# Kernel tuning notes

Measured on AMD Instinct MI355X. Metric: run time of the kernel, lower is better.

## Reference

```python
import jax, jax.numpy as jnp
import numpy as np

B, IN, H, T = 4096, 1024, 1024, 12
TIME_PENALTY = 0.01
PONDER_EPS = 0.01


def lstm_cell(x, h, c, Wih, Whh, bih, bhh):
    # PyTorch LSTMCell: gates ordered i, f, g, o
    g = x @ Wih.T + bih + h @ Whh.T + bhh  # [B, 4H]
    i, f, gg, o = jnp.split(g, 4, axis=1)
    i = jax.nn.sigmoid(i)
    f = jax.nn.sigmoid(f)
    gg = jnp.tanh(gg)
    o = jax.nn.sigmoid(o)
    c_new = f * c + i * gg
    h_new = o * jnp.tanh(c_new)
    return h_new, c_new


def setup_inputs() -> dict:
    key = jax.random.key(0)
    ks = jax.random.split(key, 12)
    k1 = 1.0 / np.sqrt(H)
    u = lambda k, shape: jax.random.uniform(k, shape, jnp.float32, -k1, k1)
    return {
        "inputs": jax.random.normal(ks[0], (B, IN), jnp.float32),
        "W_ih1": u(ks[1], (4 * H, IN + 1)),
        "W_hh1": u(ks[2], (4 * H, H)),
        "b_ih1": u(ks[3], (4 * H,)),
        "b_hh1": u(ks[4], (4 * H,)),
        "W_ih2": u(ks[5], (4 * H, H)),
        "W_hh2": u(ks[6], (4 * H, H)),
        "b_ih2": u(ks[7], (4 * H,)),
        "b_hh2": u(ks[8], (4 * H,)),
        "W_halt": u(ks[9], (1, H)),
        "b_halt": jnp.full((1,), -1.0, jnp.float32),  # initial_halting_bias
    }


def reference(inputs, W_ih1, W_hh1, b_ih1, b_hh1, W_ih2, W_hh2, b_ih2, b_hh2, W_halt, b_halt):
    batch = inputs.shape[0]
    budget = jnp.float32(1.0 - PONDER_EPS)

    h1 = jnp.zeros((batch, H), jnp.float32)
    c1 = jnp.zeros((batch, H), jnp.float32)
    h2 = jnp.zeros((batch, H), jnp.float32)
    c2 = jnp.zeros((batch, H), jnp.float32)
    halt_accum = jnp.zeros((batch, 1), jnp.float32)
    acc_out = jnp.zeros((batch, H), jnp.float32)
    acc_rem = jnp.zeros((batch, 1), jnp.float32)
    ponder_steps = jnp.zeros((batch,), jnp.float32)
    cont = jnp.ones((batch, 1), bool)
    is_first = jnp.array(True)

    def step(carry, _):
        h1, c1, h2, c2, halt_accum, acc_out, acc_rem, ponder_steps, cont, is_first = carry
        active = jnp.any(cont)  # mimic torch's early break: inactive steps are no-ops
        flag = jnp.where(is_first, 1.0, 0.0) * jnp.ones((batch, 1), jnp.float32)
        x = jnp.concatenate([inputs, flag], axis=1)
        h1n, c1n = lstm_cell(x, h1, c1, W_ih1, W_hh1, b_ih1, b_hh1)
        act = jax.nn.relu(h1n)
        h2n, c2n = lstm_cell(act, h2, c2, W_ih2, W_hh2, b_ih2, b_hh2)
        step_halt = jax.nn.sigmoid(h2n @ W_halt.T + b_halt)  # [B,1]
        cont_f = cont.astype(jnp.float32)
        masked_halt = step_halt * cont_f
        halt_n = halt_accum + masked_halt
        ending = (halt_n > budget) & cont
        cont_n = cont & jnp.logical_not(ending)
        masked_rem = ending.astype(jnp.float32) * (1.0 - halt_n)
        acc_out_n = acc_out + (masked_halt + masked_rem) * h2n
        acc_rem_n = acc_rem + masked_halt
        ponder_n = ponder_steps + cont_n[:, 0].astype(jnp.float32)
        sel = lambda new, old: jnp.where(active, new, old)
        carry_n = (sel(h1n, h1), sel(c1n, c1), sel(h2n, h2), sel(c2n, c2),
                   sel(halt_n, halt_accum), sel(acc_out_n, acc_out),
                   sel(acc_rem_n, acc_rem), sel(ponder_n, ponder_steps),
                   jnp.where(active, cont_n, cont),
                   is_first & jnp.logical_not(active))
        return carry_n, None

    carry = (h1, c1, h2, c2, halt_accum, acc_out, acc_rem, ponder_steps, cont, is_first)
    carry, _ = jax.lax.scan(step, carry, None, length=T)
    h1, c1, h2, c2, halt_accum, acc_out, acc_rem, ponder_steps, cont, _ = carry

    # for-else branch: samples still continuing after time_limit get the remainder
    acc_out = acc_out + cont.astype(jnp.float32) * (1.0 - halt_accum) * h2
    ponder_cost = -1.0 * TIME_PENALTY * jnp.mean(acc_rem)
    return acc_out, h1, c1, h2, c2, ponder_cost, ponder_steps
```

## Files before the change

kernel.cpp:

```cpp
#include <hip/hip_runtime.h>
#include <cstdint>
#include <cstddef>


typedef _Float16 f16;
typedef f16   f16x8 __attribute__((ext_vector_type(8)));
typedef f16   f16x4 __attribute__((ext_vector_type(4)));
typedef float f32x4 __attribute__((ext_vector_type(4)));

#define TSTEPS 12

#define O_ACC   0u
#define O_H1    4194304u
#define O_C1    8388608u
#define O_H2    12582912u
#define O_C2    16777216u
#define O_PCOST 20971520u
#define O_PSTEP 20971521u

#define WS_C1    (size_t)(0u)
#define WS_C2    ((size_t)16u<<20)
#define WS_H1HI0 ((size_t)32u<<20)
#define WS_H1HI1 ((size_t)40u<<20)
#define WS_H1LO0 ((size_t)48u<<20)
#define WS_H1LO1 ((size_t)56u<<20)
#define WS_H2HI0 ((size_t)64u<<20)
#define WS_H2HI1 ((size_t)72u<<20)
#define WS_H2LO0 ((size_t)80u<<20)
#define WS_H2LO1 ((size_t)88u<<20)
#define WS_ACTHI ((size_t)96u<<20)
#define WS_ACTLO ((size_t)104u<<20)
#define WS_MISC  ((size_t)112u<<20)

#define SEC_AHI 0
#define SEC_ALO 16384
#define SEC_BHI 32768
#define SEC_BLO 49152
#define BUFSZ   65536

__device__ __forceinline__ float sigmoidf_(float x) { return 1.0f / (1.0f + expf(-x)); }

__device__ __forceinline__ void glds16(const void* g, void* l) {
    __builtin_amdgcn_global_load_lds(
        (const __attribute__((address_space(1))) unsigned int*)g,
        (__attribute__((address_space(3))) unsigned int*)l, 16, 0, 0);
}

__device__ __forceinline__ void block_tile(int& m0, int& hc0) {
    const int bid = blockIdx.x;
    const int lid = (bid & 7) * 32 + (bid >> 3);
    m0  = (lid & 15) * 256;
    hc0 = (lid >> 4) * 64;
}

template<bool B_PAIR>
__device__ __forceinline__ void pass256(
    const f16* __restrict__ Ahi, const f16* __restrict__ Alo,
    const f16* __restrict__ Bhi, const f16* __restrict__ Blo,
    const float* __restrict__ Bf32,
    int m0, int hc0, f32x4 (&acc)[8][4], char* sm)
{
    const int tid = threadIdx.x, lane = tid & 63, wid = tid >> 6;
    const int wm  = (wid >> 2) * 128;
    const int wnb = wid & 3;
    const int l15 = lane & 15, lk = lane >> 4;
    const int rswz16 = (lk ^ (l15 & 3)) << 4;

    int aoff[8], boff[4];
#pragma unroll
    for (int mf = 0; mf < 8; ++mf) aoff[mf] = (wm + mf * 16 + l15) * 64 + rswz16;
#pragma unroll
    for (int nf = 0; nf < 4; ++nf) boff[nf] = (wnb * 64 + nf * 16 + l15) * 64 + rswz16;

    constexpr int NOPS = B_PAIR ? 8 : 4;
    const f16* gsrc[NOPS];
    int ldst[NOPS];
    {
        const int gl_d = lane >> 2;
        const int swzel = ((lane & 3) ^ (gl_d & 3)) * 8;
#pragma unroll
        for (int i = 0; i < NOPS; ++i) {
            const int o = wid * NOPS + i;
            const int sec = o >> 4, j = o & 15;
            const f16* base;
            size_t row;
            if (sec <= 1) { base = (sec == 0) ? Ahi : Alo; row = (size_t)(m0 + 16 * j + gl_d); }
            else {
                base = (sec == 2) ? Bhi : Blo;
                row = (size_t)((j & 3) * 1024 + hc0 + (j >> 2) * 16 + gl_d);
            }
            gsrc[i] = base + row * 1024 + swzel;
            ldst[i] = sec * 16384 + j * 1024 + lane * 16;
        }
    }

    const int blv = tid >> 1;
    const float* bsrc = nullptr;
    float4 breg[4];
    if constexpr (!B_PAIR) {
        const int wrow = ((blv >> 4) & 3) * 1024 + hc0 + (blv >> 6) * 16 + (blv & 15);
        bsrc = Bf32 + (size_t)wrow * 1024 + (tid & 1) * 16;
    }

    auto issue = [&](int i, int kt, char* buf) {
        glds16(gsrc[i] + kt * 32, buf + ldst[i]);
    };
    auto loadB = [&](int kt) {
#pragma unroll
        for (int i = 0; i < 4; ++i) breg[i] = *(const float4*)(bsrc + kt * 32 + i * 4);
    };
    auto writeB = [&](char* buf) {
#pragma unroll
        for (int i = 0; i < 4; ++i) {
            const float4 v = breg[i];
            const f16 s0 = (f16)v.x, s1 = (f16)v.y, s2 = (f16)v.z, s3 = (f16)v.w;
            const f16x4 hv = {s0, s1, s2, s3};
            const f16x4 lw = {(f16)(v.x - (float)s0), (f16)(v.y - (float)s1),
                              (f16)(v.z - (float)s2), (f16)(v.w - (float)s3)};
            const int s = (((tid & 1) * 2 + (i >> 1)) ^ (blv & 3));
            const int off = blv * 64 + (s << 4) + (i & 1) * 8;
            *(f16x4*)(buf + SEC_BHI + off) = hv;
            *(f16x4*)(buf + SEC_BLO + off) = lw;
        }
    };

    constexpr int IST_P[5] = {0, 3, 6, 8, 8};
    constexpr int IST_M[5] = {0, 2, 3, 4, 4};

#pragma unroll
    for (int i = 0; i < NOPS; ++i) issue(i, 0, sm);
    if constexpr (!B_PAIR) {
        loadB(0);
        asm volatile("s_waitcnt vmcnt(0)" ::: "memory");
        writeB(sm);
    }
    asm volatile("s_waitcnt vmcnt(0) lgkmcnt(0)" ::: "memory");
    __builtin_amdgcn_s_barrier();
    asm volatile("" ::: "memory");

    int cur = 0;
#pragma unroll 1
    for (int kt = 0; kt < 32; ++kt) {
        char* bc = sm + cur * BUFSZ;
        char* bn = sm + (cur ^ 1) * BUFSZ;
        const bool pre = (kt < 31);
        f16x8 bh[4], bl[4];
#pragma unroll
        for (int p = 0; p < 4; ++p) {
            f16x8 ah0 = *(const f16x8*)(bc + SEC_AHI + aoff[2 * p]);
            f16x8 ah1 = *(const f16x8*)(bc + SEC_AHI + aoff[2 * p + 1]);
            f16x8 al0 = *(const f16x8*)(bc + SEC_ALO + aoff[2 * p]);
            f16x8 al1 = *(const f16x8*)(bc + SEC_ALO + aoff[2 * p + 1]);
            if (p == 0) {
#pragma unroll
                for (int nf = 0; nf < 4; ++nf) {
                    bh[nf] = *(const f16x8*)(bc + SEC_BHI + boff[nf]);
                    bl[nf] = *(const f16x8*)(bc + SEC_BLO + boff[nf]);
                }
            }
            if (pre) {
                if constexpr (B_PAIR) {
#pragma unroll
                    for (int i = IST_P[p]; i < IST_P[p + 1]; ++i) issue(i, kt + 1, bn);
                } else {
#pragma unroll
                    for (int i = IST_M[p]; i < IST_M[p + 1]; ++i) issue(i, kt + 1, bn);
                    if (p == 0) loadB(kt + 1);
                }
            }
            __builtin_amdgcn_s_barrier();
#pragma unroll
            for (int i = 0; i < 2; ++i) {
                const f16x8 xh = i ? ah1 : ah0;
                const f16x8 xl = i ? al1 : al0;
#pragma unroll
                for (int nf = 0; nf < 4; ++nf) {
                    acc[2 * p + i][nf] = __builtin_amdgcn_mfma_f32_16x16x32_f16(xh, bh[nf], acc[2 * p + i][nf], 0, 0, 0);
                    acc[2 * p + i][nf] = __builtin_amdgcn_mfma_f32_16x16x32_f16(xh, bl[nf], acc[2 * p + i][nf], 0, 0, 0);
                    acc[2 * p + i][nf] = __builtin_amdgcn_mfma_f32_16x16x32_f16(xl, bh[nf], acc[2 * p + i][nf], 0, 0, 0);
                }
            }
            if (p < 3) __builtin_amdgcn_s_barrier();
        }
        asm volatile("s_waitcnt vmcnt(0)" ::: "memory");
        if constexpr (!B_PAIR) { if (pre) writeB(bn); }
        asm volatile("s_waitcnt lgkmcnt(0)" ::: "memory");
        __builtin_amdgcn_s_barrier();
        asm volatile("" ::: "memory");
        cur ^= 1;
    }
}

__global__ __launch_bounds__(512) void k_z1(
    const f16* __restrict__ xhi, const f16* __restrict__ xlo,
    const f16* __restrict__ W1hi, const f16* __restrict__ W1lo,
    const float* __restrict__ bih1, const float* __restrict__ bhh1,
    float* __restrict__ Z1)
{
    __shared__ __align__(16) char sm[2 * BUFSZ];
    int m0, hc0; block_tile(m0, hc0);
    f32x4 acc[8][4];
#pragma unroll
    for (int a = 0; a < 8; ++a)
#pragma unroll
        for (int b = 0; b < 4; ++b) acc[a][b] = (f32x4){0.f, 0.f, 0.f, 0.f};
    pass256<true>(xhi, xlo, W1hi, W1lo, nullptr, m0, hc0, acc, sm);

    const int tid = threadIdx.x, lane = tid & 63, wid = tid >> 6;
    const int wm = (wid >> 2) * 128, wnb = wid & 3, l15 = lane & 15, lk = lane >> 4;
    const int hc = hc0 + wnb * 16 + l15;
#pragma unroll
    for (int mf = 0; mf < 8; ++mf)
#pragma unroll
        for (int r = 0; r < 4; ++r) {
            const int row = m0 + wm + mf * 16 + lk * 4 + r;
#pragma unroll
            for (int g = 0; g < 4; ++g) {
                const int R = g * 1024 + hc;
                Z1[(size_t)row * 4096 + R] = acc[mf][g][r] + bih1[R] + bhh1[R];
            }
        }
}

__global__ __launch_bounds__(512) void k_stepA(
    const float* __restrict__ Z1, const float* __restrict__ Whh1,
    const f16* __restrict__ h1hi_in, const f16* __restrict__ h1lo_in,
    const float* __restrict__ flagcol, float* __restrict__ c1,
    f16* __restrict__ h1hi_out, f16* __restrict__ h1lo_out,
    f16* __restrict__ acthi, f16* __restrict__ actlo,
    const unsigned* __restrict__ cnt_prev, int step)
{
    if (step > 0 && cnt_prev[0] == 0u) return;
    __shared__ __align__(16) char sm[2 * BUFSZ];
    int m0, hc0; block_tile(m0, hc0);
    f32x4 acc[8][4];
#pragma unroll
    for (int a = 0; a < 8; ++a)
#pragma unroll
        for (int b = 0; b < 4; ++b) acc[a][b] = (f32x4){0.f, 0.f, 0.f, 0.f};
    if (step > 0)
        pass256<false>(h1hi_in, h1lo_in, nullptr, nullptr, Whh1, m0, hc0, acc, sm);

    const int tid = threadIdx.x, lane = tid & 63, wid = tid >> 6;
    const int wm = (wid >> 2) * 128, wnb = wid & 3, l15 = lane & 15, lk = lane >> 4;
    const int hc = hc0 + wnb * 16 + l15;
#pragma unroll
    for (int mf = 0; mf < 8; ++mf)
#pragma unroll
        for (int r = 0; r < 4; ++r) {
            const int row = m0 + wm + mf * 16 + lk * 4 + r;
            float p[4];
#pragma unroll
            for (int g = 0; g < 4; ++g) {
                const int R = g * 1024 + hc;
                p[g] = acc[mf][g][r] + Z1[(size_t)row * 4096 + R];
                if (step == 0) p[g] += flagcol[R];
            }
            const float ig = sigmoidf_(p[0]);
            const float fg = sigmoidf_(p[1]);
            const float gg = tanhf(p[2]);
            const float og = sigmoidf_(p[3]);
            const int idx = row * 1024 + hc;
            const float cn = fg * c1[idx] + ig * gg;
            c1[idx] = cn;
            const float h = og * tanhf(cn);
            const f16 hh = (f16)h;
            const f16 hl = (f16)(h - (float)hh);
            h1hi_out[idx] = hh; h1lo_out[idx] = hl;
            const bool pos = h > 0.0f;
            acthi[idx] = pos ? hh : (f16)0.0f;
            actlo[idx] = pos ? hl : (f16)0.0f;
        }
}

__global__ __launch_bounds__(512) void k_stepB(
    const f16* __restrict__ acthi, const f16* __restrict__ actlo,
    const float* __restrict__ Wih2,
    const f16* __restrict__ h2hi_in, const f16* __restrict__ h2lo_in,
    const float* __restrict__ Whh2,
    const float* __restrict__ bih2, const float* __restrict__ bhh2,
    float* __restrict__ c2, f16* __restrict__ h2hi_out, f16* __restrict__ h2lo_out,
    const unsigned* __restrict__ cnt_prev, int step)
{
    if (step > 0 && cnt_prev[0] == 0u) return;
    __shared__ __align__(16) char sm[2 * BUFSZ];
    int m0, hc0; block_tile(m0, hc0);
    f32x4 acc[8][4];
#pragma unroll
    for (int a = 0; a < 8; ++a)
#pragma unroll
        for (int b = 0; b < 4; ++b) acc[a][b] = (f32x4){0.f, 0.f, 0.f, 0.f};
    pass256<false>(acthi, actlo, nullptr, nullptr, Wih2, m0, hc0, acc, sm);
    if (step > 0)
        pass256<false>(h2hi_in, h2lo_in, nullptr, nullptr, Whh2, m0, hc0, acc, sm);

    const int tid = threadIdx.x, lane = tid & 63, wid = tid >> 6;
    const int wm = (wid >> 2) * 128, wnb = wid & 3, l15 = lane & 15, lk = lane >> 4;
    const int hc = hc0 + wnb * 16 + l15;
#pragma unroll
    for (int mf = 0; mf < 8; ++mf)
#pragma unroll
        for (int r = 0; r < 4; ++r) {
            const int row = m0 + wm + mf * 16 + lk * 4 + r;
            float p[4];
#pragma unroll
            for (int g = 0; g < 4; ++g) {
                const int R = g * 1024 + hc;
                p[g] = acc[mf][g][r] + bih2[R] + bhh2[R];
            }
            const float ig = sigmoidf_(p[0]);
            const float fg = sigmoidf_(p[1]);
            const float gg = tanhf(p[2]);
            const float og = sigmoidf_(p[3]);
            const int idx = row * 1024 + hc;
            const float cn = fg * c2[idx] + ig * gg;
            c2[idx] = cn;
            const float h = og * tanhf(cn);
            const f16 hh = (f16)h;
            h2hi_out[idx] = hh;
            h2lo_out[idx] = (f16)(h - (float)hh);
        }
}

__global__ __launch_bounds__(256) void k_halt(
    const f16* __restrict__ h2hi, const f16* __restrict__ h2lo,
    const float* __restrict__ Whalt, const float* __restrict__ bhalt,
    float* __restrict__ halt, float* __restrict__ cont, float* __restrict__ coef,
    float* __restrict__ ponder_out, unsigned* __restrict__ ctrl,
    const unsigned* __restrict__ cnt_prev, int step)
{
    if (step > 0 && cnt_prev[0] == 0u) return;
    const int lane = threadIdx.x & 63;
    const int b = blockIdx.x * 4 + (threadIdx.x >> 6);
    const size_t base = (size_t)b * 1024;
    float sum = 0.0f;
    for (int k = lane; k < 1024; k += 64)
        sum += ((float)h2hi[base + k] + (float)h2lo[base + k]) * Whalt[k];
#pragma unroll
    for (int off = 32; off > 0; off >>= 1) sum += __shfl_down(sum, off, 64);
    if (lane == 0) {
        const float sh = sigmoidf_(sum + bhalt[0]);
        float co = 0.0f;
        if (cont[b] != 0.0f) {
            const float hn = halt[b] + sh;
            const bool ending = hn > 0.99f;
            co = sh + (ending ? (1.0f - hn) : 0.0f);
            halt[b] = hn;
            if (!ending) {
                ponder_out[b] += 1.0f;
                atomicAdd(&ctrl[step], 1u);
            } else {
                cont[b] = 0.0f;
            }
        }
        coef[b] = co;
        if (b == 0) ctrl[12] = (unsigned)(step + 1);
    }
}

__global__ __launch_bounds__(256) void k_accum(
    const f16* __restrict__ h2hi, const f16* __restrict__ h2lo,
    const float* __restrict__ coef, float* __restrict__ acc_out,
    const unsigned* __restrict__ cnt_prev, int step)
{
    if (step > 0 && cnt_prev[0] == 0u) return;
    const int b = blockIdx.x;
    const float co = coef[b];
    if (co == 0.0f) return;
    const size_t base = (size_t)b * 1024;
    const int i = threadIdx.x;
    const f16x4 hv = *(const f16x4*)(h2hi + base + i * 4);
    const f16x4 lv = *(const f16x4*)(h2lo + base + i * 4);
    float4* dst = (float4*)(acc_out + base);
    float4 d = dst[i];
    d.x = fmaf(co, (float)hv[0] + (float)lv[0], d.x);
    d.y = fmaf(co, (float)hv[1] + (float)lv[1], d.y);
    d.z = fmaf(co, (float)hv[2] + (float)lv[2], d.z);
    d.w = fmaf(co, (float)hv[3] + (float)lv[3], d.w);
    dst[i] = d;
}

__global__ __launch_bounds__(256) void k_small_init(
    float* __restrict__ halt, float* __restrict__ cont,
    float* __restrict__ ponder_out, unsigned* __restrict__ ctrl)
{
    const int b = blockIdx.x * 256 + threadIdx.x;
    if (b < 4096) { halt[b] = 0.0f; cont[b] = 1.0f; ponder_out[b] = 0.0f; }
    if (b < 16) ctrl[b] = 0u;
}

__global__ __launch_bounds__(256) void k_split_flat(
    const float* __restrict__ src, f16* __restrict__ hi, f16* __restrict__ lo)
{
    const size_t i = ((size_t)blockIdx.x * 256 + threadIdx.x) * 4;
    const float4 v = *(const float4*)(src + i);
    const f16 s0 = (f16)v.x, s1 = (f16)v.y, s2 = (f16)v.z, s3 = (f16)v.w;
    const f16x4 hv = {s0, s1, s2, s3};
    const f16x4 lw = {(f16)(v.x - (float)s0), (f16)(v.y - (float)s1),
                      (f16)(v.z - (float)s2), (f16)(v.w - (float)s3)};
    *(f16x4*)(hi + i) = hv;
    *(f16x4*)(lo + i) = lw;
}

__global__ __launch_bounds__(256) void k_split_wih1(
    const float* __restrict__ src, f16* __restrict__ hi, f16* __restrict__ lo,
    float* __restrict__ flagcol)
{
    const int t = blockIdx.x * 256 + threadIdx.x;
    const int row = t >> 8, c4 = (t & 255) << 2;
    const float* s = src + (size_t)row * 1025 + c4;
    const float v0 = s[0], v1 = s[1], v2 = s[2], v3 = s[3];
    const f16 s0 = (f16)v0, s1 = (f16)v1, s2 = (f16)v2, s3 = (f16)v3;
    const f16x4 hv = {s0, s1, s2, s3};
    const f16x4 lw = {(f16)(v0 - (float)s0), (f16)(v1 - (float)s1),
                      (f16)(v2 - (float)s2), (f16)(v3 - (float)s3)};
    const size_t di = (size_t)row * 1024 + c4;
    *(f16x4*)(hi + di) = hv;
    *(f16x4*)(lo + di) = lw;
    if ((t & 255) == 0) flagcol[row] = src[(size_t)row * 1025 + 1024];
}

__global__ __launch_bounds__(256) void k_fin1(
    const f16* __restrict__ h1hi0, const f16* __restrict__ h1hi1,
    const f16* __restrict__ h1lo0, const f16* __restrict__ h1lo1,
    const f16* __restrict__ h2hi0, const f16* __restrict__ h2hi1,
    const f16* __restrict__ h2lo0, const f16* __restrict__ h2lo1,
    const float* __restrict__ c1s, const float* __restrict__ c2s,
    const float* __restrict__ halt, const float* __restrict__ cont,
    const unsigned* __restrict__ ctrl, float* __restrict__ out)
{
    const int par = (int)(ctrl[12] & 1u);
    const f16* h1h = par ? h1hi1 : h1hi0;
    const f16* h1l = par ? h1lo1 : h1lo0;
    const f16* h2h = par ? h2hi1 : h2hi0;
    const f16* h2l = par ? h2lo1 : h2lo0;
    const int b = blockIdx.x;
    const float rem = (cont[b] != 0.0f) ? (1.0f - halt[b]) : 0.0f;
    const int base = b * 1024;
    for (int i = threadIdx.x; i < 1024; i += 256) {
        const float h1v = (float)h1h[base + i] + (float)h1l[base + i];
        const float h2v = (float)h2h[base + i] + (float)h2l[base + i];
        out[O_H1 + base + i] = h1v;
        out[O_C1 + base + i] = c1s[base + i];
        out[O_H2 + base + i] = h2v;
        out[O_C2 + base + i] = c2s[base + i];
        if (rem != 0.0f) out[O_ACC + base + i] += rem * h2v;
    }
}

__global__ __launch_bounds__(256) void k_fin2(
    const float* __restrict__ halt, float* __restrict__ out)
{
    __shared__ float red[256];
    float s = 0.0f;
    for (int i = threadIdx.x; i < 4096; i += 256) s += halt[i];
    red[threadIdx.x] = s;
    __syncthreads();
    for (int w = 128; w > 0; w >>= 1) {
        if (threadIdx.x < w) red[threadIdx.x] += red[threadIdx.x + w];
        __syncthreads();
    }
    if (threadIdx.x == 0) out[O_PCOST] = -0.01f * (red[0] * (1.0f / 4096.0f));
}

extern "C" void kernel_launch(void* const* d_in, const int* in_sizes, int n_in,
                              void* d_out, int out_size, void* d_ws, size_t ws_size,
                              hipStream_t stream) {
    const float* inputs = (const float*)d_in[0];
    const float* W_ih1  = (const float*)d_in[1];
    const float* W_hh1  = (const float*)d_in[2];
    const float* b_ih1  = (const float*)d_in[3];
    const float* b_hh1  = (const float*)d_in[4];
    const float* W_ih2  = (const float*)d_in[5];
    const float* W_hh2  = (const float*)d_in[6];
    const float* b_ih2  = (const float*)d_in[7];
    const float* b_hh2  = (const float*)d_in[8];
    const float* W_halt = (const float*)d_in[9];
    const float* b_halt = (const float*)d_in[10];

    float* out = (float*)d_out;
    float* Z1  = out + O_H1;

    char* wsb = (char*)d_ws;
    float* c1s = (float*)(wsb + WS_C1);
    float* c2s = (float*)(wsb + WS_C2);
    f16* h1hi[2] = { (f16*)(wsb + WS_H1HI0), (f16*)(wsb + WS_H1HI1) };
    f16* h1lo[2] = { (f16*)(wsb + WS_H1LO0), (f16*)(wsb + WS_H1LO1) };
    f16* h2hi[2] = { (f16*)(wsb + WS_H2HI0), (f16*)(wsb + WS_H2HI1) };
    f16* h2lo[2] = { (f16*)(wsb + WS_H2LO0), (f16*)(wsb + WS_H2LO1) };
    f16* acthi   = (f16*)(wsb + WS_ACTHI);
    f16* actlo   = (f16*)(wsb + WS_ACTLO);
    float* halt    = (float*)(wsb + WS_MISC);
    float* cont    = halt + 4096;
    float* coef    = cont + 4096;
    float* flagcol = coef + 4096;
    unsigned* ctrl = (unsigned*)(flagcol + 4096);

    f16* xhi  = h1hi[0]; f16* xlo  = h1lo[0];
    f16* W1hi = h2hi[0]; f16* W1lo = h2lo[0];

    const size_t mb16 = (size_t)4096 * 1024 * sizeof(float);
    hipMemsetAsync(out + O_ACC, 0, mb16, stream);
    hipMemsetAsync(c1s, 0, mb16, stream);
    hipMemsetAsync(c2s, 0, mb16, stream);
    k_small_init<<<16, 256, 0, stream>>>(halt, cont, out + O_PSTEP, ctrl);

    k_split_wih1<<<4096, 256, 0, stream>>>(W_ih1, W1hi, W1lo, flagcol);
    k_split_flat<<<4096, 256, 0, stream>>>(inputs, xhi, xlo);
    k_z1<<<256, 512, 0, stream>>>(xhi, xlo, W1hi, W1lo, b_ih1, b_hh1, Z1);

    for (int s = 0; s < TSTEPS; ++s) {
        const int wsel = (s & 1) ? 0 : 1;
        const int rsel = 1 - wsel;
        const unsigned* cnt_prev = ctrl + (s > 0 ? s - 1 : 0);

        k_stepA<<<256, 512, 0, stream>>>(Z1, W_hh1, h1hi[rsel], h1lo[rsel],
                                         flagcol, c1s,
                                         h1hi[wsel], h1lo[wsel], acthi, actlo,
                                         cnt_prev, s);
        k_stepB<<<256, 512, 0, stream>>>(acthi, actlo, W_ih2,
                                         h2hi[rsel], h2lo[rsel], W_hh2,
                                         b_ih2, b_hh2, c2s,
                                         h2hi[wsel], h2lo[wsel],
                                         cnt_prev, s);
        k_halt<<<1024, 256, 0, stream>>>(h2hi[wsel], h2lo[wsel], W_halt, b_halt,
                                         halt, cont, coef, out + O_PSTEP, ctrl,
                                         cnt_prev, s);
        k_accum<<<4096, 256, 0, stream>>>(h2hi[wsel], h2lo[wsel], coef,
                                          out + O_ACC, cnt_prev, s);
    }

    k_fin1<<<4096, 256, 0, stream>>>(h1hi[0], h1hi[1], h1lo[0], h1lo[1],
                                     h2hi[0], h2hi[1], h2lo[0], h2lo[1],
                                     c1s, c2s, halt, cont, ctrl, out);
    k_fin2<<<1, 256, 0, stream>>>(halt, out);
}
```

Baseline: 1.483 ms.

## Retune LDS swizzle, widen B stores, set MFMA priority, fuse halt with accumulate

Several independent changes land together. The LDS swizzle now XORs row bits 1 and 3 to reduce bank conflicts, and the fp32-to-hi/lo split of B writes 16-byte vectors instead of 8-byte ones. MFMA blocks are wrapped in s_setprio so the compute waves get issue priority. Step 0 no longer reads c1/c2/acc_out, which removes three 16 MB memsets, and the halt and accumulate kernels are fused into one launch per step. The risk is correctness if the new swizzle does not match exactly between the global-load side and the LDS read side.

```diff
diff --git a/kernel.cpp b/kernel.cpp
--- a/kernel.cpp
+++ b/kernel.cpp
@@ -64,24 +64,31 @@
     const int wm  = (wid >> 2) * 128;
     const int wnb = wid & 3;
     const int l15 = lane & 15, lk = lane >> 4;
-    const int rswz16 = (lk ^ (l15 & 3)) << 4;
 
     int aoff[8], boff[4];
 #pragma unroll
-    for (int mf = 0; mf < 8; ++mf) aoff[mf] = (wm + mf * 16 + l15) * 64 + rswz16;
-#pragma unroll
-    for (int nf = 0; nf < 4; ++nf) boff[nf] = (wnb * 64 + nf * 16 + l15) * 64 + rswz16;
+    for (int mf = 0; mf < 8; ++mf) {
+        const int row = wm + mf * 16 + l15;
+        aoff[mf] = row * 64 + ((lk ^ (((row >> 1) ^ (row >> 3)) & 3)) << 4);
+    }
+#pragma unroll
+    for (int nf = 0; nf < 4; ++nf) {
+        const int lv = wnb * 64 + nf * 16 + l15;
+        boff[nf] = lv * 64 + ((lk ^ (((lv >> 1) ^ (lv >> 3)) & 3)) << 4);
+    }
 
     constexpr int NOPS = B_PAIR ? 8 : 4;
     const f16* gsrc[NOPS];
     int ldst[NOPS];
     {
         const int gl_d = lane >> 2;
-        const int swzel = ((lane & 3) ^ (gl_d & 3)) * 8;
+        const int sl   = lane & 3;
+        const int swz_gd = ((gl_d >> 1) ^ (gl_d >> 3)) & 3;
 #pragma unroll
         for (int i = 0; i < NOPS; ++i) {
             const int o = wid * NOPS + i;
             const int sec = o >> 4, j = o & 15;
+            const int swzv = (swz_gd ^ (2 * j)) & 3;
             const f16* base;
             size_t row;
             if (sec <= 1) { base = (sec == 0) ? Ahi : Alo; row = (size_t)(m0 + 16 * j + gl_d); }
@@ -89,12 +96,13 @@
                 base = (sec == 2) ? Bhi : Blo;
                 row = (size_t)((j & 3) * 1024 + hc0 + (j >> 2) * 16 + gl_d);
             }
-            gsrc[i] = base + row * 1024 + swzel;
+            gsrc[i] = base + row * 1024 + ((sl ^ swzv) << 3);
             ldst[i] = sec * 16384 + j * 1024 + lane * 16;
         }
     }
 
     const int blv = tid >> 1;
+    const int bswz = ((blv >> 1) ^ (blv >> 3)) & 3;
     const float* bsrc = nullptr;
     float4 breg[4];
     if constexpr (!B_PAIR) {
@@ -111,16 +119,19 @@
     };
     auto writeB = [&](char* buf) {
 #pragma unroll
-        for (int i = 0; i < 4; ++i) {
-            const float4 v = breg[i];
-            const f16 s0 = (f16)v.x, s1 = (f16)v.y, s2 = (f16)v.z, s3 = (f16)v.w;
-            const f16x4 hv = {s0, s1, s2, s3};
-            const f16x4 lw = {(f16)(v.x - (float)s0), (f16)(v.y - (float)s1),
-                              (f16)(v.z - (float)s2), (f16)(v.w - (float)s3)};
-            const int s = (((tid & 1) * 2 + (i >> 1)) ^ (blv & 3));
-            const int off = blv * 64 + (s << 4) + (i & 1) * 8;
-            *(f16x4*)(buf + SEC_BHI + off) = hv;
-            *(f16x4*)(buf + SEC_BLO + off) = lw;
+        for (int i2 = 0; i2 < 2; ++i2) {
+            const float4 va = breg[2 * i2], vb = breg[2 * i2 + 1];
+            const f16 h0 = (f16)va.x, h1 = (f16)va.y, h2 = (f16)va.z, h3 = (f16)va.w;
+            const f16 h4 = (f16)vb.x, h5 = (f16)vb.y, h6 = (f16)vb.z, h7 = (f16)vb.w;
+            const f16x8 hv = {h0, h1, h2, h3, h4, h5, h6, h7};
+            const f16x8 lw = {(f16)(va.x - (float)h0), (f16)(va.y - (float)h1),
+                              (f16)(va.z - (float)h2), (f16)(va.w - (float)h3),
+                              (f16)(vb.x - (float)h4), (f16)(vb.y - (float)h5),
+                              (f16)(vb.z - (float)h6), (f16)(vb.w - (float)h7)};
+            const int slot = ((tid & 1) * 2 + i2) ^ bswz;
+            const int off = blv * 64 + (slot << 4);
+            *(f16x8*)(buf + SEC_BHI + off) = hv;
+            *(f16x8*)(buf + SEC_BLO + off) = lw;
         }
     };
 
@@ -169,6 +180,7 @@
                 }
             }
             __builtin_amdgcn_s_barrier();
+            __builtin_amdgcn_s_setprio(1);
 #pragma unroll
             for (int i = 0; i < 2; ++i) {
                 const f16x8 xh = i ? ah1 : ah0;
@@ -180,6 +192,7 @@
                     acc[2 * p + i][nf] = __builtin_amdgcn_mfma_f32_16x16x32_f16(xl, bh[nf], acc[2 * p + i][nf], 0, 0, 0);
                 }
             }
+            __builtin_amdgcn_s_setprio(0);
             if (p < 3) __builtin_amdgcn_s_barrier();
         }
         asm volatile("s_waitcnt vmcnt(0)" ::: "memory");
@@ -261,7 +274,8 @@
             const float gg = tanhf(p[2]);
             const float og = sigmoidf_(p[3]);
             const int idx = row * 1024 + hc;
-            const float cn = fg * c1[idx] + ig * gg;
+            const float cold = (step == 0) ? 0.0f : c1[idx];
+            const float cn = fg * cold + ig * gg;
             c1[idx] = cn;
             const float h = og * tanhf(cn);
             const f16 hh = (f16)h;
@@ -313,7 +327,8 @@
             const float gg = tanhf(p[2]);
             const float og = sigmoidf_(p[3]);
             const int idx = row * 1024 + hc;
-            const float cn = fg * c2[idx] + ig * gg;
+            const float cold = (step == 0) ? 0.0f : c2[idx];
+            const float cn = fg * cold + ig * gg;
             c2[idx] = cn;
             const float h = og * tanhf(cn);
             const f16 hh = (f16)h;
@@ -322,11 +337,12 @@
         }
 }
 
-__global__ __launch_bounds__(256) void k_halt(
+__global__ __launch_bounds__(256) void k_haltacc(
     const f16* __restrict__ h2hi, const f16* __restrict__ h2lo,
     const float* __restrict__ Whalt, const float* __restrict__ bhalt,
-    float* __restrict__ halt, float* __restrict__ cont, float* __restrict__ coef,
+    float* __restrict__ halt, float* __restrict__ cont,
     float* __restrict__ ponder_out, unsigned* __restrict__ ctrl,
+    float* __restrict__ acc_out,
     const unsigned* __restrict__ cnt_prev, int step)
 {
     if (step > 0 && cnt_prev[0] == 0u) return;
@@ -338,9 +354,9 @@
         sum += ((float)h2hi[base + k] + (float)h2lo[base + k]) * Whalt[k];
 #pragma unroll
     for (int off = 32; off > 0; off >>= 1) sum += __shfl_down(sum, off, 64);
+    float co = 0.0f;
     if (lane == 0) {
         const float sh = sigmoidf_(sum + bhalt[0]);
-        float co = 0.0f;
         if (cont[b] != 0.0f) {
             const float hn = halt[b] + sh;
             const bool ending = hn > 0.99f;
@@ -353,31 +369,26 @@
                 cont[b] = 0.0f;
             }
         }
-        coef[b] = co;
         if (b == 0) ctrl[12] = (unsigned)(step + 1);
     }
-}
-
-__global__ __launch_bounds__(256) void k_accum(
-    const f16* __restrict__ h2hi, const f16* __restrict__ h2lo,
-    const float* __restrict__ coef, float* __restrict__ acc_out,
-    const unsigned* __restrict__ cnt_prev, int step)
-{
-    if (step > 0 && cnt_prev[0] == 0u) return;
-    const int b = blockIdx.x;
-    const float co = coef[b];
-    if (co == 0.0f) return;
-    const size_t base = (size_t)b * 1024;
-    const int i = threadIdx.x;
-    const f16x4 hv = *(const f16x4*)(h2hi + base + i * 4);
-    const f16x4 lv = *(const f16x4*)(h2lo + base + i * 4);
-    float4* dst = (float4*)(acc_out + base);
-    float4 d = dst[i];
-    d.x = fmaf(co, (float)hv[0] + (float)lv[0], d.x);
-    d.y = fmaf(co, (float)hv[1] + (float)lv[1], d.y);
-    d.z = fmaf(co, (float)hv[2] + (float)lv[2], d.z);
-    d.w = fmaf(co, (float)hv[3] + (float)lv[3], d.w);
-    dst[i] = d;
+    co = __shfl(co, 0, 64);
+    if (step == 0 || co != 0.0f) {
+        float4* dst = (float4*)(acc_out + base);
+        const f16x4* hi4 = (const f16x4*)(h2hi + base);
+        const f16x4* lo4 = (const f16x4*)(h2lo + base);
+#pragma unroll
+        for (int j = 0; j < 4; ++j) {
+            const int i = lane + 64 * j;
+            const f16x4 hv = hi4[i];
+            const f16x4 lv = lo4[i];
+            float4 d = (step == 0) ? (float4){0.f, 0.f, 0.f, 0.f} : dst[i];
+            d.x = fmaf(co, (float)hv[0] + (float)lv[0], d.x);
+            d.y = fmaf(co, (float)hv[1] + (float)lv[1], d.y);
+            d.z = fmaf(co, (float)hv[2] + (float)lv[2], d.z);
+            d.w = fmaf(co, (float)hv[3] + (float)lv[3], d.w);
+            dst[i] = d;
+        }
+    }
 }
 
 __global__ __launch_bounds__(256) void k_small_init(
@@ -499,10 +510,6 @@
     f16* xhi  = h1hi[0]; f16* xlo  = h1lo[0];
     f16* W1hi = h2hi[0]; f16* W1lo = h2lo[0];
 
-    const size_t mb16 = (size_t)4096 * 1024 * sizeof(float);
-    hipMemsetAsync(out + O_ACC, 0, mb16, stream);
-    hipMemsetAsync(c1s, 0, mb16, stream);
-    hipMemsetAsync(c2s, 0, mb16, stream);
     k_small_init<<<16, 256, 0, stream>>>(halt, cont, out + O_PSTEP, ctrl);
 
     k_split_wih1<<<4096, 256, 0, stream>>>(W_ih1, W1hi, W1lo, flagcol);
@@ -523,11 +530,9 @@
                                          b_ih2, b_hh2, c2s,
                                          h2hi[wsel], h2lo[wsel],
                                          cnt_prev, s);
-        k_halt<<<1024, 256, 0, stream>>>(h2hi[wsel], h2lo[wsel], W_halt, b_halt,
-                                         halt, cont, coef, out + O_PSTEP, ctrl,
-                                         cnt_prev, s);
-        k_accum<<<4096, 256, 0, stream>>>(h2hi[wsel], h2lo[wsel], coef,
-                                          out + O_ACC, cnt_prev, s);
+        k_haltacc<<<1024, 256, 0, stream>>>(h2hi[wsel], h2lo[wsel], W_halt, b_halt,
+                                            halt, cont, out + O_PSTEP, ctrl,
+                                            out + O_ACC, cnt_prev, s);
     }
 
     k_fin1<<<4096, 256, 0, stream>>>(h1hi[0], h1hi[1], h1lo[0], h1lo[1],
```

After: 1.476 ms. About the same (-0.4%).
